# Kernel tuning notes

Measured on AMD Instinct MI355X. Metric: run time of the kernel, lower is better.

The kernel has to match this reference:

```python
import jax, jax.numpy as jnp
import numpy as np

B, N, C = 2, 4096, 1024
HEADS = 16
BUCKET = 64
N_HASHES = 4
DH = C // HEADS
TOKEN_SELF_ATTN_VALUE = -5e4  # self-attention strongly discouraged (shared QK)


def setup_inputs() -> dict:
    key = jax.random.key(0)
    ks = jax.random.split(key, 8)
    s = 0.02
    n_buckets = N // BUCKET
    return {
        "queries": jax.random.normal(ks[0], (B, N, C), jnp.float32),
        "keys": jax.random.normal(ks[1], (B, N, C), jnp.float32),
        "values": jax.random.normal(ks[2], (B, N, C), jnp.float32),
        "attn_mask": jnp.zeros((1,), jnp.float32),
        "Wqk": jax.random.normal(ks[3], (C, C), jnp.float32) * s,
        "Wv": jax.random.normal(ks[4], (C, C), jnp.float32) * s,
        "Wout": jax.random.normal(ks[5], (C, C), jnp.float32) * s,
        "bout": jnp.zeros((C,), jnp.float32),
        # LSH random rotations, shared across batch and heads (reformer_pytorch default)
        "rotations": jax.random.normal(ks[6], (DH, N_HASHES, n_buckets // 2), jnp.float32),
        "tau": 1,
        "delta": 1,
    }


def _look_one_back(x):
    # concat each chunk with the previous chunk (wrap-around), along the kv axis
    extra = jnp.concatenate([x[:, -1:], x[:, :-1]], axis=1)
    return jnp.concatenate([x, extra], axis=2)


def _lsh_attention(qk, v, rotations, bucket_size, n_hashes):
    # qk, v: (bh, t, d); rotations: (d, n_hashes, n_buckets//2)
    bh, t, d = qk.shape
    n_buckets = t // bucket_size

    # --- hash vectors into buckets ---
    rotated = jnp.einsum('btf,fhi->bhti', qk, rotations)
    rotated = jnp.concatenate([rotated, -rotated], axis=-1)      # (bh, H, t, n_buckets)
    buckets = jnp.argmax(rotated, axis=-1)                       # (bh, H, t)
    offsets = (jnp.arange(n_hashes) * n_buckets)[None, :, None]
    buckets = (buckets + offsets).reshape(bh, n_hashes * t)

    # --- stable sort tokens by (bucket, position) ---
    ticker = jnp.arange(n_hashes * t)
    buckets_and_t = t * buckets + (ticker % t)[None, :]
    sticker = jnp.argsort(buckets_and_t, axis=-1)                # stable
    undo_sort = jnp.argsort(sticker, axis=-1)
    st = sticker % t                                             # original token idx per slot

    sqk = jnp.take_along_axis(qk, st[:, :, None], axis=1)
    sv = jnp.take_along_axis(v, st[:, :, None], axis=1)

    # --- chunk into n_hashes*n_buckets chunks of bucket_size ---
    n_chunks = n_hashes * n_buckets
    bq_t = st.reshape(bh, n_chunks, bucket_size)
    bqk = sqk.reshape(bh, n_chunks, bucket_size, d)
    bv = sv.reshape(bh, n_chunks, bucket_size, d)

    bq = bqk
    norm = jnp.linalg.norm(bqk, axis=-1, keepdims=True)
    bk = bqk / jnp.maximum(norm, 1e-12)                          # F.normalize, shared QK

    bk = _look_one_back(bk)
    bv = _look_one_back(bv)
    bkv_t = _look_one_back(bq_t)

    dots = jnp.einsum('bcie,bcje->bcij', bq, bk) * (d ** -0.5)   # (bh, nc, bs, 2*bs)
    self_mask = bq_t[..., :, None] == bkv_t[..., None, :]
    dots = jnp.where(self_mask, TOKEN_SELF_ATTN_VALUE, dots)

    dots_lse = jax.nn.logsumexp(dots, axis=-1, keepdims=True)
    probs = jnp.exp(dots - dots_lse)
    bo = jnp.einsum('bcij,bcje->bcie', probs, bv)

    # --- unsort and combine hash rounds by softmax over per-round logsumexps ---
    so = bo.reshape(bh, n_hashes * t, d)
    slogits = dots_lse.reshape(bh, n_hashes * t)
    o = jnp.take_along_axis(so, undo_sort[:, :, None], axis=1)
    logits = jnp.take_along_axis(slogits, undo_sort, axis=1)
    o = o.reshape(bh, n_hashes, t, d)
    logits = logits.reshape(bh, n_hashes, t, 1)
    w = jnp.exp(logits - jax.nn.logsumexp(logits, axis=1, keepdims=True))
    return jnp.sum(o * w, axis=1)                                # (bh, t, d)


def _forward(queries, Wqk, Wv, Wout, bout, rotations):
    b, n, c = queries.shape
    pad = (-n) % (BUCKET * 2)
    x = jnp.pad(queries, ((0, 0), (0, pad), (0, 0))) if pad else queries
    t = x.shape[1]
    qk = x @ Wqk.T
    v = x @ Wv.T
    qkh = qk.reshape(b, t, HEADS, DH).transpose(0, 2, 1, 3).reshape(b * HEADS, t, DH)
    vh = v.reshape(b, t, HEADS, DH).transpose(0, 2, 1, 3).reshape(b * HEADS, t, DH)
    oh = _lsh_attention(qkh, vh, rotations, BUCKET, N_HASHES)
    o = oh.reshape(b, HEADS, t, DH).transpose(0, 2, 1, 3).reshape(b, t, c)
    out = o @ Wout.T + bout
    return out[:, :n, :]


def reference(queries, keys, values, attn_mask, Wqk, Wv, Wout, bout, rotations, tau, delta):
    # keys/values/attn_mask/tau/delta are accepted but unused, as in the original layer
    return _forward(queries, Wqk, Wv, Wout, bout, rotations)
```

## Files before the change

kernel.cpp:

```cpp
#include <hip/hip_runtime.h>
#include <hip/hip_bf16.h>
#include <math.h>


#define SG_COMPUTE(BUF)                                                      \
    {                                                                        \
        _Pragma("unroll")                                                    \
        for (int kk = 0; kk < 8; ++kk) {                                     \
            float a[8], b[4];                                                \
            *(float4*)&a[0] = *(const float4*)&As[BUF][kk][tx * 4];          \
            *(float4*)&a[4] = *(const float4*)&As[BUF][kk][64 + tx * 4];     \
            *(float4*)&b[0] = *(const float4*)&Bs[BUF][kk][ty * 4];          \
            _Pragma("unroll")                                                \
            for (int i = 0; i < 8; ++i)                                      \
                _Pragma("unroll")                                            \
                for (int j = 0; j < 4; ++j)                                  \
                    acc[i][j] = fmaf(a[i], b[j], acc[i][j]);                 \
        }                                                                    \
    }

__global__ __launch_bounds__(256) void sgemm64(const float* __restrict__ A,
                                               const float* __restrict__ W,
                                               float* __restrict__ out,
                                               int headLayout,
                                               const float* __restrict__ bias) {
    __shared__ float As[2][8][128];
    __shared__ float Bs[2][8][64];
    int tid = threadIdx.x;
    int tx = tid & 15, ty = tid >> 4;
    int id = blockIdx.x;
    int swz = (id & 7) * 128 + (id >> 3);
    int tm = swz & 63;
    int tn = swz >> 6;
    int m0 = tm * 128, n0 = tn * 64;
    int lr = tid >> 1;
    int lk = (tid & 1) * 4;
    const float* pA = &A[(size_t)(m0 + lr) * 1024 + lk];
    bool doB = (tid < 128);
    int lrB = (tid & 127) >> 1;
    const float* pB = &W[(size_t)(n0 + lrB) * 1024 + lk];
    float acc[8][4];
#pragma unroll
    for (int i = 0; i < 8; ++i)
#pragma unroll
        for (int j = 0; j < 4; ++j) acc[i][j] = 0.f;

    float4 av = *(const float4*)&pA[0];
    float4 bv;
    if (doB) bv = *(const float4*)&pB[0];
    As[0][lk + 0][lr] = av.x; As[0][lk + 1][lr] = av.y;
    As[0][lk + 2][lr] = av.z; As[0][lk + 3][lr] = av.w;
    if (doB) {
        Bs[0][lk + 0][lrB] = bv.x; Bs[0][lk + 1][lrB] = bv.y;
        Bs[0][lk + 2][lrB] = bv.z; Bs[0][lk + 3][lrB] = bv.w;
    }
    __syncthreads();

    for (int it = 0; it < 127; ++it) {
        int cur = it & 1;
        int nxt = cur ^ 1;
        av = *(const float4*)&pA[(it + 1) * 8];
        if (doB) bv = *(const float4*)&pB[(it + 1) * 8];
        SG_COMPUTE(cur)
        As[nxt][lk + 0][lr] = av.x; As[nxt][lk + 1][lr] = av.y;
        As[nxt][lk + 2][lr] = av.z; As[nxt][lk + 3][lr] = av.w;
        if (doB) {
            Bs[nxt][lk + 0][lrB] = bv.x; Bs[nxt][lk + 1][lrB] = bv.y;
            Bs[nxt][lk + 2][lrB] = bv.z; Bs[nxt][lk + 3][lrB] = bv.w;
        }
        __syncthreads();
    }
    SG_COMPUTE(1)

    float4 bias4 = make_float4(0.f, 0.f, 0.f, 0.f);
    if (bias) bias4 = *(const float4*)&bias[n0 + ty * 4];
    int h = n0 >> 6;
#pragma unroll
    for (int i = 0; i < 8; ++i) {
        int m = m0 + ((i < 4) ? (tx * 4 + i) : (64 + tx * 4 + (i - 4)));
        float4 ov;
        ov.x = acc[i][0] + bias4.x;
        ov.y = acc[i][1] + bias4.y;
        ov.z = acc[i][2] + bias4.z;
        ov.w = acc[i][3] + bias4.w;
        if (headLayout) {
            int bb = m >> 12, t = m & 4095;
            *(float4*)&out[(((size_t)(bb * 16 + h)) * 4096 + t) * 64 + ty * 4] = ov;
        } else {
            *(float4*)&out[(size_t)m * 1024 + n0 + ty * 4] = ov;
        }
    }
}
#undef SG_COMPUTE

__global__ __launch_bounds__(256) void bucket32(const float* __restrict__ qk,
                                                const float* __restrict__ rot,
                                                int* __restrict__ keys) {
    int tid = threadIdx.x;
    int blk = blockIdx.x;
    int token = (blk & 15) * 256 + tid;
    int r = (blk >> 4) & 3;
    int bh = blk >> 6;
    const float* q = &qk[((size_t)bh * 4096 + token) * 64];
    float racc[32];
#pragma unroll
    for (int i = 0; i < 32; ++i) racc[i] = 0.f;
    for (int f0 = 0; f0 < 64; f0 += 4) {
        float4 qv = *(const float4*)&q[f0];
        const float* rp0 = &rot[(f0 + 0) * 128 + r * 32];
        const float* rp1 = rp0 + 128;
        const float* rp2 = rp0 + 256;
        const float* rp3 = rp0 + 384;
#pragma unroll
        for (int i = 0; i < 32; ++i) racc[i] = fmaf(qv.x, rp0[i], racc[i]);
#pragma unroll
        for (int i = 0; i < 32; ++i) racc[i] = fmaf(qv.y, rp1[i], racc[i]);
#pragma unroll
        for (int i = 0; i < 32; ++i) racc[i] = fmaf(qv.z, rp2[i], racc[i]);
#pragma unroll
        for (int i = 0; i < 32; ++i) racc[i] = fmaf(qv.w, rp3[i], racc[i]);
    }
    float best = -INFINITY;
    int bi = 0;
#pragma unroll
    for (int i = 0; i < 32; ++i) { if (racc[i] > best) { best = racc[i]; bi = i; } }
#pragma unroll
    for (int i = 0; i < 32; ++i) { float x = -racc[i]; if (x > best) { best = x; bi = 32 + i; } }
    int bin = r * 64 + bi;
    keys[(size_t)bh * 16384 + r * 4096 + token] = bin * 4096 + token;
}

#define PST 257

__global__ __launch_bounds__(256) void countsort_kernel(const int* __restrict__ keys,
                                                        int* __restrict__ st_sorted) {
    __shared__ unsigned short pre[64 * PST];
    __shared__ unsigned char sbin[4096];
    __shared__ unsigned short sperm[4096];
    __shared__ int qsum[64 * 4];
    __shared__ int qoff[64 * 4];
    __shared__ int binOffset[64];

    int tid = threadIdx.x;
    int bh = blockIdx.x >> 2;
    int r = blockIdx.x & 3;
    const int* kb = &keys[(((size_t)bh * 4 + r) << 12)];

    for (int u = tid; u < 64 * PST; u += 256) pre[u] = 0;
    __syncthreads();

    int base = tid << 4;
#pragma unroll
    for (int u = 0; u < 4; ++u) {
        int4 kv = *(const int4*)&kb[base + u * 4];
        int b0 = (kv.x >> 12) & 63;
        int b1 = (kv.y >> 12) & 63;
        int b2 = (kv.z >> 12) & 63;
        int b3 = (kv.w >> 12) & 63;
        sbin[base + u * 4 + 0] = (unsigned char)b0;
        sbin[base + u * 4 + 1] = (unsigned char)b1;
        sbin[base + u * 4 + 2] = (unsigned char)b2;
        sbin[base + u * 4 + 3] = (unsigned char)b3;
        pre[b0 * PST + tid]++;
        pre[b1 * PST + tid]++;
        pre[b2 * PST + tid]++;
        pre[b3 * PST + tid]++;
    }
    __syncthreads();

    int b = tid & 63, q = tid >> 6;
    {
        int run = 0;
        for (int i = 0; i < 64; ++i) run += pre[b * PST + q * 64 + i];
        qsum[b * 4 + q] = run;
    }
    __syncthreads();

    if (tid < 64) {
        int s0 = qsum[tid * 4 + 0], s1 = qsum[tid * 4 + 1];
        int s2 = qsum[tid * 4 + 2], s3 = qsum[tid * 4 + 3];
        qoff[tid * 4 + 0] = 0;
        qoff[tid * 4 + 1] = s0;
        qoff[tid * 4 + 2] = s0 + s1;
        qoff[tid * 4 + 3] = s0 + s1 + s2;
        binOffset[tid] = s0 + s1 + s2 + s3;
    }
    __syncthreads();
    if (tid == 0) {
        int running = 0;
        for (int i = 0; i < 64; ++i) {
            int t = binOffset[i];
            binOffset[i] = running;
            running += t;
        }
    }
    __syncthreads();

    {
        int run2 = qoff[b * 4 + q];
        for (int i = 0; i < 64; ++i) {
            int idx = b * PST + q * 64 + i;
            int t = pre[idx];
            pre[idx] = (unsigned short)run2;
            run2 += t;
        }
    }
    __syncthreads();

#pragma unroll
    for (int k = 0; k < 16; ++k) {
        int bin = sbin[base + k];
        int off = pre[bin * PST + tid]++;
        sperm[binOffset[bin] + off] = (unsigned short)(base + k);
    }
    __syncthreads();

    int* ob = &st_sorted[(((size_t)bh * 4 + r) << 12)];
#pragma unroll
    for (int u = 0; u < 16; ++u) ob[u * 256 + tid] = (int)sperm[u * 256 + tid];
}

__global__ __launch_bounds__(256) void attn_kernel(const float* __restrict__ qk,
                                                   const float* __restrict__ v,
                                                   const int* __restrict__ st_sorted,
                                                   float* __restrict__ o4,
                                                   float* __restrict__ lse4) {
    __shared__ float bufA[128 * 68];
    __shared__ float red[64 * 17];
    __shared__ int posl[128];
    __shared__ int voff[128];
    __shared__ float invl[128];

    int tid = threadIdx.x;
    int bh = blockIdx.x >> 8;
    int c = blockIdx.x & 255;
    int r = c >> 6;
    int pc = (c + 255) & 255;
    const int* stb = &st_sorted[(size_t)bh * 16384];
    if (tid < 64) {
        int p = stb[c * 64 + tid];
        posl[tid] = p;
        voff[tid] = p << 8;
    } else if (tid < 128) {
        int p = stb[pc * 64 + (tid - 64)];
        posl[tid] = p;
        voff[tid] = p << 8;
    }
    __syncthreads();

    float* kqt = bufA;
#pragma unroll
    for (int u = 0; u < 8; ++u) {
        int flat = u * 256 + tid;
        int row = flat >> 4;
        int f4 = (flat & 15) * 4;
        size_t gbase = ((size_t)bh * 4096 + posl[row]) * 64 + f4;
        float4 qv = *(const float4*)&qk[gbase];
        int rw = row ^ ((((f4 >> 2)) & 7) << 2);
        kqt[(f4 + 0) * 132 + rw] = qv.x;
        kqt[(f4 + 1) * 132 + rw] = qv.y;
        kqt[(f4 + 2) * 132 + rw] = qv.z;
        kqt[(f4 + 3) * 132 + rw] = qv.w;
    }
    __syncthreads();

    if (tid < 128) {
        float ss = 0.f;
        for (int f = 0; f < 64; ++f) {
            int s = ((f >> 2) & 7) << 2;
            float x = kqt[f * 132 + (tid ^ s)];
            ss += x * x;
        }
        invl[tid] = 1.0f / fmaxf(sqrtf(ss), 1e-12f);
    }
    __syncthreads();

    int tx = tid & 15, ty = tid >> 4;
    float acc[4][8];
#pragma unroll
    for (int i = 0; i < 4; ++i)
#pragma unroll
        for (int j = 0; j < 8; ++j) acc[i][j] = 0.f;
#pragma unroll
    for (int f = 0; f < 64; ++f) {
        int s = ((f >> 2) & 7) << 2;
        float a[4], b[8];
        *(float4*)a = *(const float4*)&kqt[f * 132 + ((tx * 4) ^ s)];
        *(float4*)&b[0] = *(const float4*)&kqt[f * 132 + ((ty * 8) ^ s)];
        *(float4*)&b[4] = *(const float4*)&kqt[f * 132 + ((ty * 8 + 4) ^ s)];
#pragma unroll
        for (int i = 0; i < 4; ++i)
#pragma unroll
            for (int j = 0; j < 8; ++j) acc[i][j] = fmaf(a[i], b[j], acc[i][j]);
    }

    int qp[4];
#pragma unroll
    for (int ii = 0; ii < 4; ++ii) qp[ii] = posl[tx * 4 + ii];
#pragma unroll
    for (int jj = 0; jj < 8; ++jj) {
        int j = ty * 8 + jj;
        float sc = invl[j] * 0.125f;
        int kp = posl[j];
#pragma unroll
        for (int ii = 0; ii < 4; ++ii) {
            float x = acc[ii][jj] * sc;
            acc[ii][jj] = (qp[ii] == kp) ? -5e4f : x;
        }
    }

#pragma unroll
    for (int ii = 0; ii < 4; ++ii) {
        float pm = acc[ii][0];
#pragma unroll
        for (int jj = 1; jj < 8; ++jj) pm = fmaxf(pm, acc[ii][jj]);
        red[(tx * 4 + ii) * 17 + ty] = pm;
    }
    __syncthreads();
    float m[4];
#pragma unroll
    for (int ii = 0; ii < 4; ++ii) {
        float mm = red[(tx * 4 + ii) * 17 + 0];
        for (int t = 1; t < 16; ++t) mm = fmaxf(mm, red[(tx * 4 + ii) * 17 + t]);
        m[ii] = mm;
    }
    __syncthreads();

    float* pT = bufA;
    float ps[4] = {0.f, 0.f, 0.f, 0.f};
#pragma unroll
    for (int jj = 0; jj < 8; ++jj) {
        int j = ty * 8 + jj;
        float e0 = __expf(acc[0][jj] - m[0]);
        float e1 = __expf(acc[1][jj] - m[1]);
        float e2 = __expf(acc[2][jj] - m[2]);
        float e3 = __expf(acc[3][jj] - m[3]);
        ps[0] += e0; ps[1] += e1; ps[2] += e2; ps[3] += e3;
        float4 ev; ev.x = e0; ev.y = e1; ev.z = e2; ev.w = e3;
        *(float4*)&pT[j * 68 + tx * 4] = ev;
    }
#pragma unroll
    for (int ii = 0; ii < 4; ++ii) red[(tx * 4 + ii) * 17 + ty] = ps[ii];
    __syncthreads();
    float l[4];
#pragma unroll
    for (int ii = 0; ii < 4; ++ii) {
        float s = 0.f;
        for (int t = 0; t < 16; ++t) s += red[(tx * 4 + ii) * 17 + t];
        l[ii] = s;
    }

    if (ty == 0) {
#pragma unroll
        for (int ii = 0; ii < 4; ++ii) {
            int i = tx * 4 + ii;
            lse4[((size_t)bh * 4 + r) * 4096 + posl[i]] = m[ii] + __logf(l[ii]);
        }
    }

    const char* vb8 = (const char*)v + ((size_t)bh << 20);
    int coff = ty * 16;
    float acc2[4][4];
#pragma unroll
    for (int i = 0; i < 4; ++i)
#pragma unroll
        for (int j = 0; j < 4; ++j) acc2[i][j] = 0.f;

    float4 p0 = *(const float4*)(vb8 + (voff[0] + coff));
    float4 p1 = *(const float4*)(vb8 + (voff[1] + coff));
    float4 p2 = *(const float4*)(vb8 + (voff[2] + coff));
    float4 p3 = *(const float4*)(vb8 + (voff[3] + coff));
    for (int j0 = 0; j0 < 128; j0 += 4) {
        float4 c0 = p0, c1 = p1, c2 = p2, c3 = p3;
        if (j0 + 4 < 128) {
            p0 = *(const float4*)(vb8 + (voff[j0 + 4] + coff));
            p1 = *(const float4*)(vb8 + (voff[j0 + 5] + coff));
            p2 = *(const float4*)(vb8 + (voff[j0 + 6] + coff));
            p3 = *(const float4*)(vb8 + (voff[j0 + 7] + coff));
        }
#define PVSTEP(JJ, CV)                                                       \
        {                                                                    \
            float a_[4];                                                     \
            *(float4*)a_ = *(const float4*)&pT[(j0 + (JJ)) * 68 + tx * 4];   \
            acc2[0][0] = fmaf(a_[0], CV.x, acc2[0][0]);                      \
            acc2[0][1] = fmaf(a_[0], CV.y, acc2[0][1]);                      \
            acc2[0][2] = fmaf(a_[0], CV.z, acc2[0][2]);                      \
            acc2[0][3] = fmaf(a_[0], CV.w, acc2[0][3]);                      \
            acc2[1][0] = fmaf(a_[1], CV.x, acc2[1][0]);                      \
            acc2[1][1] = fmaf(a_[1], CV.y, acc2[1][1]);                      \
            acc2[1][2] = fmaf(a_[1], CV.z, acc2[1][2]);                      \
            acc2[1][3] = fmaf(a_[1], CV.w, acc2[1][3]);                      \
            acc2[2][0] = fmaf(a_[2], CV.x, acc2[2][0]);                      \
            acc2[2][1] = fmaf(a_[2], CV.y, acc2[2][1]);                      \
            acc2[2][2] = fmaf(a_[2], CV.z, acc2[2][2]);                      \
            acc2[2][3] = fmaf(a_[2], CV.w, acc2[2][3]);                      \
            acc2[3][0] = fmaf(a_[3], CV.x, acc2[3][0]);                      \
            acc2[3][1] = fmaf(a_[3], CV.y, acc2[3][1]);                      \
            acc2[3][2] = fmaf(a_[3], CV.z, acc2[3][2]);                      \
            acc2[3][3] = fmaf(a_[3], CV.w, acc2[3][3]);                      \
        }
        PVSTEP(0, c0)
        PVSTEP(1, c1)
        PVSTEP(2, c2)
        PVSTEP(3, c3)
#undef PVSTEP
    }
#pragma unroll
    for (int ii = 0; ii < 4; ++ii) {
        int i = tx * 4 + ii;
        float rl = 1.0f / l[ii];
        size_t ob = (((size_t)bh * 4 + r) * 4096 + posl[i]) * 64 + ty * 4;
        float4 ov;
        ov.x = acc2[ii][0] * rl;
        ov.y = acc2[ii][1] * rl;
        ov.z = acc2[ii][2] * rl;
        ov.w = acc2[ii][3] * rl;
        *(float4*)&o4[ob] = ov;
    }
}

__global__ __launch_bounds__(256) void combine_kernel(const float* __restrict__ o4,
                                                      const float* __restrict__ lse4,
                                                      float* __restrict__ o_bt) {
    int tid = threadIdx.x;
    int gt = blockIdx.x * 4 + (tid >> 6);
    int d = tid & 63;
    int bh = gt >> 12, p = gt & 4095;
    size_t base = ((size_t)bh * 4) * 4096 + p;
    float l0 = lse4[base];
    float l1 = lse4[base + 4096];
    float l2 = lse4[base + 8192];
    float l3 = lse4[base + 12288];
    float mm = fmaxf(fmaxf(l0, l1), fmaxf(l2, l3));
    float w0 = __expf(l0 - mm), w1 = __expf(l1 - mm);
    float w2 = __expf(l2 - mm), w3 = __expf(l3 - mm);
    float W = w0 + w1 + w2 + w3;
    size_t ob = (((size_t)bh * 4) * 4096 + p) * 64 + d;
    const size_t rs = (size_t)4096 * 64;
    float o = w0 * o4[ob]
            + w1 * o4[ob + rs]
            + w2 * o4[ob + 2 * rs]
            + w3 * o4[ob + 3 * rs];
    int b = bh >> 4, h = bh & 15;
    o_bt[((size_t)b * 4096 + p) * 1024 + h * 64 + d] = o / W;
}

extern "C" void kernel_launch(void* const* d_in, const int* in_sizes, int n_in,
                              void* d_out, int out_size, void* d_ws, size_t ws_size,
                              hipStream_t stream) {
    const float* x    = (const float*)d_in[0];
    const float* Wqk  = (const float*)d_in[4];
    const float* Wv   = (const float*)d_in[5];
    const float* Wout = (const float*)d_in[6];
    const float* bout = (const float*)d_in[7];
    const float* rot  = (const float*)d_in[8];
    float* out = (float*)d_out;

    char* ws = (char*)d_ws;
    float* qk32          = (float*)(ws);
    float* v             = (float*)(ws + 33554432);
    float* o4            = (float*)(ws + 67108864);
    float* lse4          = (float*)(ws + 201326592);
    int* keys            = (int*)(ws + 203423744);
    int* st_sorted       = (int*)(ws + 205520896);
    float* o_bt          = qk32;

    sgemm64<<<1024, 256, 0, stream>>>(x, Wqk, qk32, 1, nullptr);
    sgemm64<<<1024, 256, 0, stream>>>(x, Wv, v, 1, nullptr);
    bucket32<<<2048, 256, 0, stream>>>(qk32, rot, keys);
    countsort_kernel<<<128, 256, 0, stream>>>(keys, st_sorted);
    attn_kernel<<<8192, 256, 0, stream>>>(qk32, v, st_sorted, o4, lse4);
    combine_kernel<<<32768, 256, 0, stream>>>(o4, lse4, o_bt);
    sgemm64<<<1024, 256, 0, stream>>>(o_bt, Wout, out, 0, bout);
}
```

Baseline: 1.213 ms.

## Enlarge SGEMM tiles to 128x128 and fuse QK and V projections into one launch

The GEMM tile grows from 128x64 to 128x128, so each thread computes an 8x8 accumulator block instead of 8x4. This raises FMA work per shared-memory load and cuts redundant global reads of A. The QK and V projections are merged into one 1024-block launch that picks the weight matrix by column tile, and the output projection uses 512 larger blocks. The cost is more registers per thread, which may lower occupancy, and fewer blocks for the output GEMM.

```diff
diff --git a/kernel.cpp b/kernel.cpp
--- a/kernel.cpp
+++ b/kernel.cpp
@@ -7,91 +7,138 @@
     {                                                                        \
         _Pragma("unroll")                                                    \
         for (int kk = 0; kk < 8; ++kk) {                                     \
-            float a[8], b[4];                                                \
+            float a[8], b[8];                                                \
             *(float4*)&a[0] = *(const float4*)&As[BUF][kk][tx * 4];          \
             *(float4*)&a[4] = *(const float4*)&As[BUF][kk][64 + tx * 4];     \
             *(float4*)&b[0] = *(const float4*)&Bs[BUF][kk][ty * 4];          \
+            *(float4*)&b[4] = *(const float4*)&Bs[BUF][kk][64 + ty * 4];     \
             _Pragma("unroll")                                                \
             for (int i = 0; i < 8; ++i)                                      \
                 _Pragma("unroll")                                            \
-                for (int j = 0; j < 4; ++j)                                  \
+                for (int j = 0; j < 8; ++j)                                  \
                     acc[i][j] = fmaf(a[i], b[j], acc[i][j]);                 \
         }                                                                    \
     }
 
-__global__ __launch_bounds__(256) void sgemm64(const float* __restrict__ A,
-                                               const float* __restrict__ W,
-                                               float* __restrict__ out,
-                                               int headLayout,
-                                               const float* __restrict__ bias) {
+#define SG_STAGE(BUF)                                                        \
+    {                                                                        \
+        As[BUF][lk + 0][lr] = av.x; As[BUF][lk + 1][lr] = av.y;              \
+        As[BUF][lk + 2][lr] = av.z; As[BUF][lk + 3][lr] = av.w;              \
+        Bs[BUF][lk + 0][lr] = bv.x; Bs[BUF][lk + 1][lr] = bv.y;              \
+        Bs[BUF][lk + 2][lr] = bv.z; Bs[BUF][lk + 3][lr] = bv.w;              \
+    }
+
+__global__ __launch_bounds__(256) void proj2(const float* __restrict__ A,
+                                             const float* __restrict__ Wqk,
+                                             const float* __restrict__ Wv,
+                                             float* __restrict__ outQK,
+                                             float* __restrict__ outV) {
     __shared__ float As[2][8][128];
-    __shared__ float Bs[2][8][64];
+    __shared__ float Bs[2][8][128];
     int tid = threadIdx.x;
     int tx = tid & 15, ty = tid >> 4;
     int id = blockIdx.x;
     int swz = (id & 7) * 128 + (id >> 3);
-    int tm = swz & 63;
-    int tn = swz >> 6;
-    int m0 = tm * 128, n0 = tn * 64;
+    int tm = swz >> 4;
+    int tn = swz & 15;
+    int m0 = tm * 128;
+    const float* Wsel = (tn < 8) ? Wqk : Wv;
+    float* dst = (tn < 8) ? outQK : outV;
+    int nsel = (tn & 7) * 128;
     int lr = tid >> 1;
     int lk = (tid & 1) * 4;
     const float* pA = &A[(size_t)(m0 + lr) * 1024 + lk];
-    bool doB = (tid < 128);
-    int lrB = (tid & 127) >> 1;
-    const float* pB = &W[(size_t)(n0 + lrB) * 1024 + lk];
-    float acc[8][4];
+    const float* pB = &Wsel[(size_t)(nsel + lr) * 1024 + lk];
+    float acc[8][8];
 #pragma unroll
     for (int i = 0; i < 8; ++i)
 #pragma unroll
-        for (int j = 0; j < 4; ++j) acc[i][j] = 0.f;
+        for (int j = 0; j < 8; ++j) acc[i][j] = 0.f;
 
     float4 av = *(const float4*)&pA[0];
-    float4 bv;
-    if (doB) bv = *(const float4*)&pB[0];
-    As[0][lk + 0][lr] = av.x; As[0][lk + 1][lr] = av.y;
-    As[0][lk + 2][lr] = av.z; As[0][lk + 3][lr] = av.w;
-    if (doB) {
-        Bs[0][lk + 0][lrB] = bv.x; Bs[0][lk + 1][lrB] = bv.y;
-        Bs[0][lk + 2][lrB] = bv.z; Bs[0][lk + 3][lrB] = bv.w;
-    }
+    float4 bv = *(const float4*)&pB[0];
+    SG_STAGE(0)
     __syncthreads();
 
     for (int it = 0; it < 127; ++it) {
         int cur = it & 1;
         int nxt = cur ^ 1;
         av = *(const float4*)&pA[(it + 1) * 8];
-        if (doB) bv = *(const float4*)&pB[(it + 1) * 8];
+        bv = *(const float4*)&pB[(it + 1) * 8];
         SG_COMPUTE(cur)
-        As[nxt][lk + 0][lr] = av.x; As[nxt][lk + 1][lr] = av.y;
-        As[nxt][lk + 2][lr] = av.z; As[nxt][lk + 3][lr] = av.w;
-        if (doB) {
-            Bs[nxt][lk + 0][lrB] = bv.x; Bs[nxt][lk + 1][lrB] = bv.y;
-            Bs[nxt][lk + 2][lrB] = bv.z; Bs[nxt][lk + 3][lrB] = bv.w;
-        }
+        SG_STAGE(nxt)
         __syncthreads();
     }
     SG_COMPUTE(1)
 
-    float4 bias4 = make_float4(0.f, 0.f, 0.f, 0.f);
-    if (bias) bias4 = *(const float4*)&bias[n0 + ty * 4];
-    int h = n0 >> 6;
+    int h0 = nsel >> 6;
 #pragma unroll
     for (int i = 0; i < 8; ++i) {
         int m = m0 + ((i < 4) ? (tx * 4 + i) : (64 + tx * 4 + (i - 4)));
-        float4 ov;
-        ov.x = acc[i][0] + bias4.x;
-        ov.y = acc[i][1] + bias4.y;
-        ov.z = acc[i][2] + bias4.z;
-        ov.w = acc[i][3] + bias4.w;
-        if (headLayout) {
-            int bb = m >> 12, t = m & 4095;
-            *(float4*)&out[(((size_t)(bb * 16 + h)) * 4096 + t) * 64 + ty * 4] = ov;
-        } else {
-            *(float4*)&out[(size_t)m * 1024 + n0 + ty * 4] = ov;
-        }
+        int bb = m >> 12, t = m & 4095;
+        float4 o0, o1;
+        o0.x = acc[i][0]; o0.y = acc[i][1]; o0.z = acc[i][2]; o0.w = acc[i][3];
+        o1.x = acc[i][4]; o1.y = acc[i][5]; o1.z = acc[i][6]; o1.w = acc[i][7];
+        *(float4*)&dst[(((size_t)(bb * 16 + h0)) * 4096 + t) * 64 + ty * 4] = o0;
+        *(float4*)&dst[(((size_t)(bb * 16 + h0 + 1)) * 4096 + t) * 64 + ty * 4] = o1;
+    }
+}
+
+__global__ __launch_bounds__(256) void sgemm_out(const float* __restrict__ A,
+                                                 const float* __restrict__ W,
+                                                 float* __restrict__ out,
+                                                 const float* __restrict__ bias) {
+    __shared__ float As[2][8][128];
+    __shared__ float Bs[2][8][128];
+    int tid = threadIdx.x;
+    int tx = tid & 15, ty = tid >> 4;
+    int id = blockIdx.x;
+    int swz = (id & 7) * 64 + (id >> 3);
+    int tm = swz >> 3;
+    int tn = swz & 7;
+    int m0 = tm * 128, n0 = tn * 128;
+    int lr = tid >> 1;
+    int lk = (tid & 1) * 4;
+    const float* pA = &A[(size_t)(m0 + lr) * 1024 + lk];
+    const float* pB = &W[(size_t)(n0 + lr) * 1024 + lk];
+    float acc[8][8];
+#pragma unroll
+    for (int i = 0; i < 8; ++i)
+#pragma unroll
+        for (int j = 0; j < 8; ++j) acc[i][j] = 0.f;
+
+    float4 av = *(const float4*)&pA[0];
+    float4 bv = *(const float4*)&pB[0];
+    SG_STAGE(0)
+    __syncthreads();
+
+    for (int it = 0; it < 127; ++it) {
+        int cur = it & 1;
+        int nxt = cur ^ 1;
+        av = *(const float4*)&pA[(it + 1) * 8];
+        bv = *(const float4*)&pB[(it + 1) * 8];
+        SG_COMPUTE(cur)
+        SG_STAGE(nxt)
+        __syncthreads();
+    }
+    SG_COMPUTE(1)
+
+    float4 bias0 = *(const float4*)&bias[n0 + ty * 4];
+    float4 bias1 = *(const float4*)&bias[n0 + 64 + ty * 4];
+#pragma unroll
+    for (int i = 0; i < 8; ++i) {
+        int m = m0 + ((i < 4) ? (tx * 4 + i) : (64 + tx * 4 + (i - 4)));
+        float4 o0, o1;
+        o0.x = acc[i][0] + bias0.x; o0.y = acc[i][1] + bias0.y;
+        o0.z = acc[i][2] + bias0.z; o0.w = acc[i][3] + bias0.w;
+        o1.x = acc[i][4] + bias1.x; o1.y = acc[i][5] + bias1.y;
+        o1.z = acc[i][6] + bias1.z; o1.w = acc[i][7] + bias1.w;
+        *(float4*)&out[(size_t)m * 1024 + n0 + ty * 4] = o0;
+        *(float4*)&out[(size_t)m * 1024 + n0 + 64 + ty * 4] = o1;
     }
 }
 #undef SG_COMPUTE
+#undef SG_STAGE
 
 __global__ __launch_bounds__(256) void bucket32(const float* __restrict__ qk,
                                                 const float* __restrict__ rot,
@@ -465,11 +512,10 @@
     int* st_sorted       = (int*)(ws + 205520896);
     float* o_bt          = qk32;
 
-    sgemm64<<<1024, 256, 0, stream>>>(x, Wqk, qk32, 1, nullptr);
-    sgemm64<<<1024, 256, 0, stream>>>(x, Wv, v, 1, nullptr);
+    proj2<<<1024, 256, 0, stream>>>(x, Wqk, Wv, qk32, v);
     bucket32<<<2048, 256, 0, stream>>>(qk32, rot, keys);
     countsort_kernel<<<128, 256, 0, stream>>>(keys, st_sorted);
     attn_kernel<<<8192, 256, 0, stream>>>(qk32, v, st_sorted, o4, lse4);
     combine_kernel<<<32768, 256, 0, stream>>>(o4, lse4, o_bt);
-    sgemm64<<<1024, 256, 0, stream>>>(o_bt, Wout, out, 0, bout);
-}
+    sgemm_out<<<512, 256, 0, stream>>>(o_bt, Wout, out, bout);
+}
```

Measured after the change: 1.090 ms. 10.1% less time.
